# Optimization experiments

Hardware: AMD Instinct MI355X
Metric: run time of the kernel (lower is better)

Reference implementation:

```python
import jax, jax.numpy as jnp
import numpy as np

N_NODES = 50000
N_EDGES = 800000
IN_DIM = 16
H1, H2, H3, HFC = 64, 128, 256, 256


def setup_inputs() -> dict:
    key = jax.random.key(0)
    ks = jax.random.split(key, 8)
    w = lambda k, s: jax.random.normal(k, s, dtype=jnp.float32) * 0.05
    return {
        "X": jax.random.normal(ks[0], (N_NODES, IN_DIM), dtype=jnp.float32),
        "edge_index": jax.random.randint(ks[1], (2, N_EDGES), 0, N_NODES, dtype=jnp.int64),
        "W1": w(ks[2], (2 * IN_DIM, H1)), "b1": jnp.zeros((H1,), jnp.float32),
        "W2": w(ks[3], (2 * H1, H2)), "b2": jnp.zeros((H2,), jnp.float32),
        "W3": w(ks[4], (2 * H2, H3)), "b3": jnp.zeros((H3,), jnp.float32),
        "Wf1": w(ks[5], (H3, HFC)), "bf1": jnp.zeros((HFC,), jnp.float32),
        "Wf2": w(ks[6], (HFC, 1)), "bf2": jnp.zeros((1,), jnp.float32),
    }


def edge_conv(x, edge_index, W, b):
    # EdgeConv (DGCNN): msg = ReLU(Linear([x_i, x_j - x_i])), max-aggregate at i
    src, dst = edge_index[0], edge_index[1]
    xi = x[dst]                      # [E, d] target node feats
    xj = x[src]                      # [E, d] source node feats
    msg = jax.nn.relu(jnp.concatenate([xi, xj - xi], axis=-1) @ W + b)  # [E, out]
    agg = jax.ops.segment_max(msg, dst, num_segments=x.shape[0])        # [N, out]
    # nodes with no incoming edge get -inf from segment_max -> zero them
    return jnp.where(jnp.isneginf(agg), 0.0, agg)


def reference(X, edge_index, W1, b1, W2, b2, W3, b3, Wf1, bf1, Wf2, bf2):
    H = edge_conv(X, edge_index, W1, b1)
    H = edge_conv(H, edge_index, W2, b2)
    H = edge_conv(H, edge_index, W3, b3)
    # MLP head (dropout is identity at inference)
    H = jax.nn.relu(H @ Wf1 + bf1)
    out = jax.nn.sigmoid(H @ Wf2 + bf2)
    return out.squeeze(-1)  # [N]
```

## Files before the change

### kernel.cpp

```cpp
#include <hip/hip_runtime.h>
#include <math.h>

#define NN 50000
#define NE 800000

typedef unsigned short ushort_t;
typedef __attribute__((ext_vector_type(8))) short bf16x8;
typedef __attribute__((ext_vector_type(4))) float f32x4;

__device__ inline unsigned short f2bf(float f) {
    unsigned int u = __float_as_uint(f);
    u = (u + 0x7fffu + ((u >> 16) & 1u)) >> 16;
    return (unsigned short)u;
}
__device__ inline unsigned int pack2bf(float lo, float hi) {
    return (unsigned int)f2bf(lo) | ((unsigned int)f2bf(hi) << 16);
}

__global__ void prep0_kernel(const int* __restrict__ ei, int istride,
                             int* __restrict__ esrc32, int* __restrict__ edst32,
                             int* __restrict__ deg) {
    int i = blockIdx.x * blockDim.x + threadIdx.x;
    int s = gridDim.x * blockDim.x;
    for (int j = i; j < NN; j += s) deg[j] = 0;
    const int* eis = ei;
    const int* eid = ei + (size_t)NE * istride;
    for (int j = i; j < NE; j += s) {
        esrc32[j] = eis[(size_t)j * istride];
        edst32[j] = eid[(size_t)j * istride];
    }
}

__global__ void hist_kernel(const int* __restrict__ edst, int* __restrict__ deg, int nE) {
    int i = blockIdx.x * blockDim.x + threadIdx.x;
    int s = gridDim.x * blockDim.x;
    for (; i < nE; i += s) atomicAdd(&deg[edst[i]], 1);
}

__global__ __launch_bounds__(256)
void scan_reduce(const int* __restrict__ deg, int* __restrict__ bsum, int n) {
    __shared__ int s[256];
    const int t = threadIdx.x;
    const int i = blockIdx.x * 256 + t;
    s[t] = (i < n) ? deg[i] : 0;
    __syncthreads();
#pragma unroll
    for (int off = 128; off > 0; off >>= 1) {
        if (t < off) s[t] += s[t + off];
        __syncthreads();
    }
    if (t == 0) bsum[blockIdx.x] = s[0];
}

__global__ __launch_bounds__(256)
void scan_tops(const int* __restrict__ bsum, int* __restrict__ boff,
               int* __restrict__ rowptr, int nb, int n) {
    __shared__ int s[256];
    const int t = threadIdx.x;
    const int v = (t < nb) ? bsum[t] : 0;
    s[t] = v;
    __syncthreads();
    for (int off = 1; off < 256; off <<= 1) {
        int u = (t >= off) ? s[t - off] : 0;
        __syncthreads();
        s[t] += u;
        __syncthreads();
    }
    if (t < nb) boff[t] = s[t] - v;
    if (t == 255) rowptr[n] = s[255];
}

__global__ __launch_bounds__(256)
void scan_apply(int* __restrict__ deg, const int* __restrict__ boff,
                int* __restrict__ rowptr, int n) {
    __shared__ int s[256];
    const int t = threadIdx.x;
    const int i = blockIdx.x * 256 + t;
    const int v = (i < n) ? deg[i] : 0;
    s[t] = v;
    __syncthreads();
    for (int off = 1; off < 256; off <<= 1) {
        int u = (t >= off) ? s[t - off] : 0;
        __syncthreads();
        s[t] += u;
        __syncthreads();
    }
    if (i < n) {
        int ex = boff[blockIdx.x] + s[t] - v;
        rowptr[i] = ex;
        deg[i] = ex;
    }
}

__global__ void scatter_kernel(const int* __restrict__ esrc, const int* __restrict__ edst,
                               int* __restrict__ cursor, int* __restrict__ col, int nE) {
    int i = blockIdx.x * blockDim.x + threadIdx.x;
    int s = gridDim.x * blockDim.x;
    for (; i < nE; i += s) {
        int d = edst[i];
        int pos = atomicAdd(&cursor[d], 1);
        col[pos] = esrc[i];
    }
}

__global__ void megaprep_kernel(const float* __restrict__ W1, const float* __restrict__ W2,
                                const float* __restrict__ W3, const float* __restrict__ Wf1,
                                const float* __restrict__ X,
                                ushort_t* __restrict__ Wt1, ushort_t* __restrict__ Wt2,
                                ushort_t* __restrict__ Wt3, ushort_t* __restrict__ Wf1t,
                                ushort_t* __restrict__ Xb, float* __restrict__ hacc) {
    const int T0 = 128 * 32;
    const int T1 = T0 + 256 * 64;
    const int T2 = T1 + 512 * 128;
    const int T3 = T2 + 256 * 256;
    const int T4 = T3 + NN * 32;
    const int T5 = T4 + NN;
    int i = blockIdx.x * blockDim.x + threadIdx.x;
    int s = gridDim.x * blockDim.x;
    for (; i < T5; i += s) {
        if (i < T0) {
            int idx = i, o = idx / 32, k = idx % 32;
            float v = 0.f;
            if (k < 16)
                v = (o < 64) ? (W1[k * 64 + o] - W1[(k + 16) * 64 + o])
                             : W1[(k + 16) * 64 + (o - 64)];
            Wt1[idx] = f2bf(v);
        } else if (i < T1) {
            int idx = i - T0, o = idx / 64, k = idx % 64;
            float v = (o < 128) ? (W2[k * 128 + o] - W2[(k + 64) * 128 + o])
                                : W2[(k + 64) * 128 + (o - 128)];
            Wt2[idx] = f2bf(v);
        } else if (i < T2) {
            int idx = i - T1, o = idx / 128, k = idx % 128;
            float v = (o < 256) ? (W3[(size_t)k * 256 + o] - W3[(size_t)(k + 128) * 256 + o])
                                : W3[(size_t)(k + 128) * 256 + (o - 256)];
            Wt3[idx] = f2bf(v);
        } else if (i < T3) {
            int idx = i - T2, nn = idx / 256, k = idx % 256;
            Wf1t[idx] = f2bf(Wf1[(size_t)k * 256 + nn]);
        } else if (i < T4) {
            int idx = i - T3, row = idx >> 5, c = idx & 31;
            Xb[idx] = (c < 16) ? f2bf(X[(size_t)row * 16 + c]) : (ushort_t)0;
        } else {
            hacc[i - T4] = 0.f;
        }
    }
}

template<int K, int OUT, int NF, int MR>
__global__ __launch_bounds__(256)
void gemm_mfma(const ushort_t* __restrict__ A, const ushort_t* __restrict__ Wt,
               const float* __restrict__ bias, ushort_t* __restrict__ PQ, int n) {
    constexpr int NOUT = 2 * OUT;
    constexpr int KB = K / 32;
    const int wave = threadIdx.x >> 6;
    const int lane = threadIdx.x & 63;
    const int lr = lane & 15;
    const int kg = lane >> 4;
    const int row0 = (blockIdx.x * 4 + wave) * (MR * 16);
    const int col0 = blockIdx.y * (NF * 16);

    f32x4 acc[MR][NF];
#pragma unroll
    for (int m = 0; m < MR; ++m)
#pragma unroll
        for (int f = 0; f < NF; ++f) acc[m][f] = (f32x4)(0.f);

    const ushort_t* Ap[MR];
#pragma unroll
    for (int m = 0; m < MR; ++m) {
        int arow = row0 + m * 16 + lr;
        if (arow >= n) arow = n - 1;
        Ap[m] = A + (size_t)arow * K + kg * 8;
    }
    const ushort_t* Bp = Wt + (size_t)(col0 + lr) * K + kg * 8;

#pragma unroll
    for (int kb = 0; kb < KB; ++kb) {
        bf16x8 af[MR];
#pragma unroll
        for (int m = 0; m < MR; ++m) af[m] = *(const bf16x8*)(Ap[m] + kb * 32);
        bf16x8 bfv[NF];
#pragma unroll
        for (int f = 0; f < NF; ++f)
            bfv[f] = *(const bf16x8*)(Bp + (size_t)f * 16 * K + kb * 32);
#pragma unroll
        for (int f = 0; f < NF; ++f)
#pragma unroll
            for (int m = 0; m < MR; ++m)
                acc[m][f] = __builtin_amdgcn_mfma_f32_16x16x32_bf16(af[m], bfv[f], acc[m][f], 0, 0, 0);
    }

#pragma unroll
    for (int m = 0; m < MR; ++m) {
#pragma unroll
        for (int f = 0; f < NF; ++f) {
            int c = col0 + f * 16 + lr;
            float bb = (c < OUT) ? bias[c] : 0.f;
#pragma unroll
            for (int r = 0; r < 4; ++r) {
                int row = row0 + m * 16 + kg * 4 + r;
                if (row < n) PQ[(size_t)row * NOUT + c] = f2bf(acc[m][f][r] + bb);
            }
        }
    }
}

__global__ __launch_bounds__(256)
void head_mfma(const ushort_t* __restrict__ H, const ushort_t* __restrict__ Wf1t,
               const float* __restrict__ bf1, const float* __restrict__ Wf2,
               float* __restrict__ hacc, int n) {
    const int wave = threadIdx.x >> 6;
    const int lane = threadIdx.x & 63;
    const int row0 = (blockIdx.x * 4 + wave) * 16;
    const int col0 = blockIdx.y * 128;
    const int lr = lane & 15;
    const int kg = lane >> 4;

    f32x4 acc[8];
#pragma unroll
    for (int i = 0; i < 8; ++i) acc[i] = (f32x4)(0.f);

    int arow = row0 + lr;
    if (arow >= n) arow = n - 1;
    const ushort_t* Aptr = H + (size_t)arow * 256 + kg * 8;
    const ushort_t* Bp = Wf1t + (size_t)(col0 + lr) * 256 + kg * 8;

#pragma unroll
    for (int kb = 0; kb < 8; ++kb) {
        bf16x8 afrag = *(const bf16x8*)(Aptr + kb * 32);
        bf16x8 bfv[8];
#pragma unroll
        for (int nf = 0; nf < 8; ++nf)
            bfv[nf] = *(const bf16x8*)(Bp + (size_t)nf * 16 * 256 + kb * 32);
#pragma unroll
        for (int nf = 0; nf < 8; ++nf)
            acc[nf] = __builtin_amdgcn_mfma_f32_16x16x32_bf16(afrag, bfv[nf], acc[nf], 0, 0, 0);
    }

    float part[4] = {0.f, 0.f, 0.f, 0.f};
#pragma unroll
    for (int nf = 0; nf < 8; ++nf) {
        int c = col0 + nf * 16 + lr;
        float w2 = Wf2[c];
        float bb = bf1[c];
#pragma unroll
        for (int r = 0; r < 4; ++r)
            part[r] = fmaf(fmaxf(acc[nf][r] + bb, 0.f), w2, part[r]);
    }
#pragma unroll
    for (int s = 1; s < 16; s <<= 1) {
#pragma unroll
        for (int r = 0; r < 4; ++r) part[r] += __shfl_xor(part[r], s, 16);
    }
    if (lr == 0) {
#pragma unroll
        for (int r = 0; r < 4; ++r) {
            int row = row0 + kg * 4 + r;
            if (row < n) atomicAdd(&hacc[row], part[r]);
        }
    }
}

__global__ void sigmoid_kernel(const float* __restrict__ hacc, const float* __restrict__ bf2,
                               float* __restrict__ out, int n) {
    int i = blockIdx.x * blockDim.x + threadIdx.x;
    int s = gridDim.x * blockDim.x;
    float b = bf2[0];
    for (; i < n; i += s) out[i] = 1.f / (1.f + expf(-(hacc[i] + b)));
}

template<int OUT>
__global__ __launch_bounds__(256, 8)
void segmax_combine(const ushort_t* __restrict__ PQ, const int* __restrict__ rowptr,
                    const int* __restrict__ col, ushort_t* __restrict__ Hout, int n) {
    constexpr int NOUT = 2 * OUT;
    constexpr int G = OUT / 8;
    constexpr int NPB = 256 / G;
    const int gid = threadIdx.x / G;
    const int lane = threadIdx.x % G;
    const int i = blockIdx.x * NPB + gid;
    if (i >= n) return;

    const int r0 = rowptr[i];
    const int r1 = rowptr[i + 1];
    const int c8 = lane * 8;

    float m[8];
#pragma unroll
    for (int j = 0; j < 8; ++j) m[j] = -INFINITY;

    auto domax = [&](uint4 q) {
        m[0] = fmaxf(m[0], __uint_as_float(q.x << 16));
        m[1] = fmaxf(m[1], __uint_as_float(q.x & 0xffff0000u));
        m[2] = fmaxf(m[2], __uint_as_float(q.y << 16));
        m[3] = fmaxf(m[3], __uint_as_float(q.y & 0xffff0000u));
        m[4] = fmaxf(m[4], __uint_as_float(q.z << 16));
        m[5] = fmaxf(m[5], __uint_as_float(q.z & 0xffff0000u));
        m[6] = fmaxf(m[6], __uint_as_float(q.w << 16));
        m[7] = fmaxf(m[7], __uint_as_float(q.w & 0xffff0000u));
    };

    int r = r0;
    for (; r + 3 < r1; r += 4) {
        int s0 = col[r], s1 = col[r + 1], s2 = col[r + 2], s3 = col[r + 3];
        uint4 q0 = *(const uint4*)(PQ + (size_t)s0 * NOUT + OUT + c8);
        uint4 q1 = *(const uint4*)(PQ + (size_t)s1 * NOUT + OUT + c8);
        uint4 q2 = *(const uint4*)(PQ + (size_t)s2 * NOUT + OUT + c8);
        uint4 q3 = *(const uint4*)(PQ + (size_t)s3 * NOUT + OUT + c8);
        domax(q0); domax(q1); domax(q2); domax(q3);
    }
    for (; r < r1; ++r) {
        domax(*(const uint4*)(PQ + (size_t)col[r] * NOUT + OUT + c8));
    }

    const uint4 pb = *(const uint4*)(PQ + (size_t)i * NOUT + c8);
    float p[8];
    p[0] = __uint_as_float(pb.x << 16); p[1] = __uint_as_float(pb.x & 0xffff0000u);
    p[2] = __uint_as_float(pb.y << 16); p[3] = __uint_as_float(pb.y & 0xffff0000u);
    p[4] = __uint_as_float(pb.z << 16); p[5] = __uint_as_float(pb.z & 0xffff0000u);
    p[6] = __uint_as_float(pb.w << 16); p[7] = __uint_as_float(pb.w & 0xffff0000u);

    float h[8];
#pragma unroll
    for (int j = 0; j < 8; ++j) h[j] = fmaxf(p[j] + m[j], 0.f);

    uint4 o;
    o.x = pack2bf(h[0], h[1]);
    o.y = pack2bf(h[2], h[3]);
    o.z = pack2bf(h[4], h[5]);
    o.w = pack2bf(h[6], h[7]);
    *(uint4*)(Hout + (size_t)i * OUT + c8) = o;
}

extern "C" void kernel_launch(void* const* d_in, const int* in_sizes, int n_in,
                              void* d_out, int out_size, void* d_ws, size_t ws_size,
                              hipStream_t stream) {
    const float* X   = (const float*)d_in[0];
    const int*   ei  = (const int*)d_in[1];
    const float* W1  = (const float*)d_in[2];
    const float* b1  = (const float*)d_in[3];
    const float* W2  = (const float*)d_in[4];
    const float* b2  = (const float*)d_in[5];
    const float* W3  = (const float*)d_in[6];
    const float* b3  = (const float*)d_in[7];
    const float* Wf1 = (const float*)d_in[8];
    const float* bf1 = (const float*)d_in[9];
    const float* Wf2 = (const float*)d_in[10];
    const float* bf2 = (const float*)d_in[11];
    float* out = (float*)d_out;

    int istride = (in_sizes[1] == 4 * NE) ? 2 : 1;

    ushort_t* PQ     = (ushort_t*)d_ws;
    ushort_t* Ha     = PQ + (size_t)NN * 512;
    ushort_t* Hb     = Ha + (size_t)NN * 256;
    int*      rowptr = (int*)(Hb + (size_t)NN * 256);
    int*      deg    = rowptr + (NN + 8);
    int*      col    = deg + NN;
    int*      esrc32 = col + NE;
    int*      edst32 = esrc32 + NE;
    int*      bsum   = edst32 + NE;
    int*      boff   = bsum + 256;
    ushort_t* Wt1    = (ushort_t*)(boff + 256);
    ushort_t* Wt2    = Wt1 + 128 * 32;
    ushort_t* Wt3    = Wt2 + 256 * 64;
    ushort_t* Wf1t   = Wt3 + 512 * 128;
    ushort_t* Xb     = Wf1t + 256 * 256;
    float*    hacc   = (float*)(Xb + (size_t)NN * 32);

    const int NB = (NN + 255) / 256;

    prep0_kernel<<<1024, 256, 0, stream>>>(ei, istride, esrc32, edst32, deg);
    hist_kernel<<<1024, 256, 0, stream>>>(edst32, deg, NE);
    scan_reduce<<<NB, 256, 0, stream>>>(deg, bsum, NN);
    scan_tops<<<1, 256, 0, stream>>>(bsum, boff, rowptr, NB, NN);
    scan_apply<<<NB, 256, 0, stream>>>(deg, boff, rowptr, NN);
    scatter_kernel<<<1024, 256, 0, stream>>>(esrc32, edst32, deg, col, NE);

    megaprep_kernel<<<1024, 256, 0, stream>>>(W1, W2, W3, Wf1, X,
                                              Wt1, Wt2, Wt3, Wf1t, Xb, hacc);

    const int GB = (NN + 127) / 128;

    {
        dim3 g(GB, 1);
        gemm_mfma<32, 64, 8, 2><<<g, 256, 0, stream>>>(Xb, Wt1, b1, PQ, NN);
    }
    segmax_combine<64><<<(NN + 31) / 32, 256, 0, stream>>>(PQ, rowptr, col, Ha, NN);

    {
        dim3 g(GB, 2);
        gemm_mfma<64, 128, 8, 2><<<g, 256, 0, stream>>>(Ha, Wt2, b2, PQ, NN);
    }
    segmax_combine<128><<<(NN + 15) / 16, 256, 0, stream>>>(PQ, rowptr, col, Hb, NN);

    {
        dim3 g(GB, 4);
        gemm_mfma<128, 256, 8, 2><<<g, 256, 0, stream>>>(Hb, Wt3, b3, PQ, NN);
    }
    segmax_combine<256><<<(NN + 7) / 8, 256, 0, stream>>>(PQ, rowptr, col, Ha, NN);

    {
        dim3 g((NN + 63) / 64, 2);
        head_mfma<<<g, 256, 0, stream>>>(Ha, Wf1t, bf1, Wf2, hacc, NN);
    }
    sigmoid_kernel<<<64, 256, 0, stream>>>(hacc, bf2, out, NN);
}
```

Measured before the change: 377.0 us.

## Stage GEMM output through LDS for coalesced stores and double-buffer fragment loads

The GEMM epilogue now writes bf16 results into a shared-memory tile and then stores whole rows with 16-byte coalesced writes, replacing scattered 2-byte stores. Both the GEMM and head kernels prefetch the next K-slice's A/B fragments into registers while issuing MFMAs on the current slice, and launch bounds now request minimum occupancy. The changes target store inefficiency and load latency, at the cost of more registers and an LDS tile. The LDS tile assumes 128 rows by 128 columns per block, which must match the template parameters.

```diff
diff --git a/kernel.cpp b/kernel.cpp
--- a/kernel.cpp
+++ b/kernel.cpp
@@ -148,16 +148,19 @@
 }
 
 template<int K, int OUT, int NF, int MR>
-__global__ __launch_bounds__(256)
+__global__ __launch_bounds__(256, 3)
 void gemm_mfma(const ushort_t* __restrict__ A, const ushort_t* __restrict__ Wt,
                const float* __restrict__ bias, ushort_t* __restrict__ PQ, int n) {
     constexpr int NOUT = 2 * OUT;
     constexpr int KB = K / 32;
+    __shared__ ushort_t lds[128][132];
+
     const int wave = threadIdx.x >> 6;
     const int lane = threadIdx.x & 63;
     const int lr = lane & 15;
     const int kg = lane >> 4;
-    const int row0 = (blockIdx.x * 4 + wave) * (MR * 16);
+    const int row0b = blockIdx.x * (4 * MR * 16);
+    const int row0 = row0b + wave * (MR * 16);
     const int col0 = blockIdx.y * (NF * 16);
 
     f32x4 acc[MR][NF];
@@ -175,38 +178,61 @@
     }
     const ushort_t* Bp = Wt + (size_t)(col0 + lr) * K + kg * 8;
 
+    bf16x8 af[2][MR];
+    bf16x8 bfv[2][NF];
+#pragma unroll
+    for (int m = 0; m < MR; ++m) af[0][m] = *(const bf16x8*)(Ap[m]);
+#pragma unroll
+    for (int f = 0; f < NF; ++f) bfv[0][f] = *(const bf16x8*)(Bp + (size_t)f * 16 * K);
+
 #pragma unroll
     for (int kb = 0; kb < KB; ++kb) {
-        bf16x8 af[MR];
-#pragma unroll
-        for (int m = 0; m < MR; ++m) af[m] = *(const bf16x8*)(Ap[m] + kb * 32);
-        bf16x8 bfv[NF];
+        const int cur = kb & 1, nxt = cur ^ 1;
+        if (kb + 1 < KB) {
+#pragma unroll
+            for (int m = 0; m < MR; ++m)
+                af[nxt][m] = *(const bf16x8*)(Ap[m] + (kb + 1) * 32);
+#pragma unroll
+            for (int f = 0; f < NF; ++f)
+                bfv[nxt][f] = *(const bf16x8*)(Bp + (size_t)f * 16 * K + (kb + 1) * 32);
+        }
 #pragma unroll
         for (int f = 0; f < NF; ++f)
-            bfv[f] = *(const bf16x8*)(Bp + (size_t)f * 16 * K + kb * 32);
-#pragma unroll
-        for (int f = 0; f < NF; ++f)
 #pragma unroll
             for (int m = 0; m < MR; ++m)
-                acc[m][f] = __builtin_amdgcn_mfma_f32_16x16x32_bf16(af[m], bfv[f], acc[m][f], 0, 0, 0);
+                acc[m][f] = __builtin_amdgcn_mfma_f32_16x16x32_bf16(af[cur][m], bfv[cur][f], acc[m][f], 0, 0, 0);
     }
 
 #pragma unroll
     for (int m = 0; m < MR; ++m) {
 #pragma unroll
         for (int f = 0; f < NF; ++f) {
-            int c = col0 + f * 16 + lr;
-            float bb = (c < OUT) ? bias[c] : 0.f;
+            int cg = col0 + f * 16 + lr;
+            float bb = (cg < OUT) ? bias[cg] : 0.f;
 #pragma unroll
             for (int r = 0; r < 4; ++r) {
-                int row = row0 + m * 16 + kg * 4 + r;
-                if (row < n) PQ[(size_t)row * NOUT + c] = f2bf(acc[m][f][r] + bb);
+                lds[wave * (MR * 16) + m * 16 + kg * 4 + r][f * 16 + lr] =
+                    f2bf(acc[m][f][r] + bb);
             }
         }
     }
-}
-
-__global__ __launch_bounds__(256)
+    __syncthreads();
+
+    const int t = threadIdx.x;
+#pragma unroll
+    for (int it = 0; it < 8; ++it) {
+        int j = it * 256 + t;
+        int row = j >> 4;
+        int q = j & 15;
+        int grow = row0b + row;
+        if (grow < n) {
+            uint4 v = *(const uint4*)(&lds[row][q * 8]);
+            *(uint4*)(PQ + (size_t)grow * NOUT + col0 + q * 8) = v;
+        }
+    }
+}
+
+__global__ __launch_bounds__(256, 4)
 void head_mfma(const ushort_t* __restrict__ H, const ushort_t* __restrict__ Wf1t,
                const float* __restrict__ bf1, const float* __restrict__ Wf2,
                float* __restrict__ hacc, int n) {
@@ -226,16 +252,23 @@
     const ushort_t* Aptr = H + (size_t)arow * 256 + kg * 8;
     const ushort_t* Bp = Wf1t + (size_t)(col0 + lr) * 256 + kg * 8;
 
+    bf16x8 afb[2], bfb[2][8];
+    afb[0] = *(const bf16x8*)(Aptr);
+#pragma unroll
+    for (int nf = 0; nf < 8; ++nf) bfb[0][nf] = *(const bf16x8*)(Bp + (size_t)nf * 16 * 256);
+
 #pragma unroll
     for (int kb = 0; kb < 8; ++kb) {
-        bf16x8 afrag = *(const bf16x8*)(Aptr + kb * 32);
-        bf16x8 bfv[8];
+        const int cur = kb & 1, nxt = cur ^ 1;
+        if (kb + 1 < 8) {
+            afb[nxt] = *(const bf16x8*)(Aptr + (kb + 1) * 32);
+#pragma unroll
+            for (int nf = 0; nf < 8; ++nf)
+                bfb[nxt][nf] = *(const bf16x8*)(Bp + (size_t)nf * 16 * 256 + (kb + 1) * 32);
+        }
 #pragma unroll
         for (int nf = 0; nf < 8; ++nf)
-            bfv[nf] = *(const bf16x8*)(Bp + (size_t)nf * 16 * 256 + kb * 32);
-#pragma unroll
-        for (int nf = 0; nf < 8; ++nf)
-            acc[nf] = __builtin_amdgcn_mfma_f32_16x16x32_bf16(afrag, bfv[nf], acc[nf], 0, 0, 0);
+            acc[nf] = __builtin_amdgcn_mfma_f32_16x16x32_bf16(afb[cur], bfb[cur][nf], acc[nf], 0, 0, 0);
     }
 
     float part[4] = {0.f, 0.f, 0.f, 0.f};
```

New measurement: 349.0 us. 7.4% less time.
